# Kernel tuning notes

Hardware: AMD Instinct MI355X
Metric: run time of the kernel (lower is better)

Reference implementation:

```python
import jax, jax.numpy as jnp
import numpy as np

B, T, D = 2, 2048, 1024
H = 16
DH = D // H


def setup_inputs() -> dict:
    key = jax.random.key(0)
    ks = jax.random.split(key, 6)
    s = 1.0 / np.sqrt(D)
    return {
        "input_emb": jax.random.normal(ks[0], (B, T, D), dtype=jnp.float32),
        "W_key": jax.random.normal(ks[1], (D, D), dtype=jnp.float32) * s,
        "W_query": jax.random.normal(ks[2], (D, D), dtype=jnp.float32) * s,
        "W_value": jax.random.normal(ks[3], (D, D), dtype=jnp.float32) * s,
        "W_out": jax.random.normal(ks[4], (D, D), dtype=jnp.float32) * s,
        "b_out": jnp.zeros((D,), dtype=jnp.float32),
    }


def reference(input_emb, W_key, W_query, W_value, W_out, b_out):
    b, t, _ = input_emb.shape
    # projections (no bias on K/Q/V, matching bias_on=False)
    k = (input_emb @ W_key).reshape(b, t, H, DH).transpose(0, 2, 1, 3)    # [b,h,t,dh]
    q = (input_emb @ W_query).reshape(b, t, H, DH).transpose(0, 2, 1, 3)
    v = (input_emb @ W_value).reshape(b, t, H, DH).transpose(0, 2, 1, 3)
    # NOTE: source computes K @ Q^T (not Q @ K^T) — reproduce faithfully.
    scores = jnp.einsum("bhid,bhjd->bhij", k, q) / jnp.sqrt(jnp.float32(DH))
    mask = jnp.triu(jnp.ones((t, t), dtype=bool), k=1)                    # True where j > i
    scores = jnp.where(mask, -jnp.inf, scores)
    attn = jax.nn.softmax(scores, axis=-1)                                # softmax over j (query axis)
    ctx = jnp.einsum("bhij,bhjd->bhid", attn, v)                          # [b,h,t,dh]
    ctx = ctx.transpose(0, 2, 1, 3).reshape(b, t, H * DH)                 # [b,t,d]
    return ctx @ W_out + b_out
```

## Files before the change

kernel.cpp:

```cpp
#include <hip/hip_runtime.h>
#include <cstdint>
#include <cstddef>

#define T_SEQ 2048
#define DMODEL 1024
#define NHEAD 16
#define DHEAD 64
#define BATCH 2
#define MROWS (BATCH * T_SEQ)

typedef __attribute__((ext_vector_type(8))) short bf16x8;
typedef __attribute__((ext_vector_type(4))) float f32x4;
typedef unsigned int u32;

__device__ __forceinline__ unsigned short f2bf(float f) {
  u32 u = __float_as_uint(f);
  u32 r = (u + 0x7FFFu + ((u >> 16) & 1u)) >> 16;
  return (unsigned short)r;
}

__device__ __forceinline__ u32 cvtpk(float a, float b) {
  u32 r;
  asm("v_cvt_pk_bf16_f32 %0, %1, %2" : "=v"(r) : "v"(a), "v"(b));
  return r;
}

__device__ __forceinline__ void gl_lds16(const unsigned short* g, unsigned short* l) {
  __builtin_amdgcn_global_load_lds(
      (const __attribute__((address_space(1))) u32*)g,
      (__attribute__((address_space(3))) u32*)l, 16, 0, 0);
}

__global__ void k_prep(const float* __restrict__ X, unsigned short* __restrict__ Xb,
                       const float* __restrict__ W0, const float* __restrict__ W1,
                       const float* __restrict__ W2, const float* __restrict__ W3,
                       unsigned short* __restrict__ T0, unsigned short* __restrict__ T1,
                       unsigned short* __restrict__ T2, unsigned short* __restrict__ T3) {
  const int bid = blockIdx.x;
  if (bid < 4096) {
    int i = (bid * 256 + threadIdx.x) * 4;
    float4 v = *reinterpret_cast<const float4*>(X + i);
    ushort4 o;
    o.x = f2bf(v.x); o.y = f2bf(v.y); o.z = f2bf(v.z); o.w = f2bf(v.w);
    *reinterpret_cast<ushort4*>(Xb + i) = o;
    return;
  }
  const int b2 = bid - 4096;
  const int z = b2 >> 10;
  const int rem = b2 & 1023;
  const int cx = rem & 31, ry = rem >> 5;
  const float* W = (z == 0) ? W0 : (z == 1) ? W1 : (z == 2) ? W2 : W3;
  unsigned short* Wt = (z == 0) ? T0 : (z == 1) ? T1 : (z == 2) ? T2 : T3;
  __shared__ float tile[32][33];
  const int c0 = cx * 32, r0 = ry * 32;
  const int tx = threadIdx.x & 31, ty = threadIdx.x >> 5;
#pragma unroll
  for (int i = ty; i < 32; i += 8)
    tile[i][tx] = W[(size_t)(r0 + i) * DMODEL + c0 + tx];
  __syncthreads();
#pragma unroll
  for (int i = ty; i < 32; i += 8)
    Wt[(size_t)(c0 + i) * DMODEL + r0 + tx] = f2bf(tile[tx][i]);
}

__global__ __launch_bounds__(256, 2)
void k_gemm_qkv(const unsigned short* __restrict__ Xb,
                const unsigned short* __restrict__ Wkt,
                const unsigned short* __restrict__ Wqt,
                const unsigned short* __restrict__ Wvt,
                unsigned short* __restrict__ Qr,
                unsigned short* __restrict__ Kr,
                unsigned short* __restrict__ Vt)
{
  __shared__ __align__(16) unsigned short As[3][128 * 32];
  __shared__ __align__(16) unsigned short Bs[3][128 * 32];
  const int orig = blockIdx.x;
  const int t = (orig & 7) * 96 + (orig >> 3);
  const int z = t >> 8;
  const int remt = t & 255;
  const int by = remt >> 3, bx = remt & 7;
  const unsigned short* Bt = (z == 0) ? Wkt : (z == 1) ? Wqt : Wvt;

  const int tid = threadIdx.x;
  const int lane = tid & 63, w = tid >> 6;
  const int wr = w >> 1, wc = w & 1;
  const int l15 = lane & 15, l4 = lane >> 4;
  const int m0 = by * 128, n0 = bx * 128;

  const int srow = tid >> 2, scc = tid & 3;
  const unsigned short* Ab0 = Xb + (size_t)(m0 + srow) * DMODEL + scc * 8;
  const unsigned short* Bb0 = Bt + (size_t)(n0 + srow) * DMODEL + scc * 8;
  const unsigned short* Ab1 = Ab0 + (size_t)64 * DMODEL;
  const unsigned short* Bb1 = Bb0 + (size_t)64 * DMODEL;

#define GSTAGE(buf, koff)                                                 \
  {                                                                       \
    gl_lds16(Ab0 + (koff), As[buf] + tid * 8);                            \
    gl_lds16(Ab1 + (koff), As[buf] + 2048 + tid * 8);                     \
    gl_lds16(Bb0 + (koff), Bs[buf] + tid * 8);                            \
    gl_lds16(Bb1 + (koff), Bs[buf] + 2048 + tid * 8);                     \
  }

#define GCOMP(buf)                                                        \
  {                                                                       \
    bf16x8 af[4], bfr[4];                                                 \
    _Pragma("unroll")                                                     \
    for (int mi = 0; mi < 4; ++mi)                                        \
      af[mi] = *reinterpret_cast<const bf16x8*>(As[buf] + (wr * 64 + mi * 16 + l15) * 32 + l4 * 8); \
    _Pragma("unroll")                                                     \
    for (int ni = 0; ni < 4; ++ni)                                        \
      bfr[ni] = *reinterpret_cast<const bf16x8*>(Bs[buf] + (wc * 64 + ni * 16 + l15) * 32 + l4 * 8); \
    __builtin_amdgcn_s_setprio(1);                                        \
    _Pragma("unroll")                                                     \
    for (int mi = 0; mi < 4; ++mi)                                        \
      _Pragma("unroll")                                                   \
      for (int ni = 0; ni < 4; ++ni)                                      \
        acc[mi][ni] = __builtin_amdgcn_mfma_f32_16x16x32_bf16(af[mi], bfr[ni], acc[mi][ni], 0, 0, 0); \
    __builtin_amdgcn_s_setprio(0);                                        \
  }

#define SB __builtin_amdgcn_sched_barrier(0);
#define GW4 asm volatile("s_waitcnt vmcnt(4)" ::: "memory");
#define GW0 asm volatile("s_waitcnt vmcnt(0)" ::: "memory");

#define GSTEP(P, NB)                                                      \
  SB GW4 SB __builtin_amdgcn_s_barrier(); SB                              \
  if (ko < DMODEL) { GSTAGE(NB, ko) ko += 32; }                           \
  GCOMP(P)

  f32x4 acc[4][4] = {};

  GSTAGE(0, 0)
  GSTAGE(1, 32)
  int ko = 64;
  for (int j = 0; j < 10; ++j) {
    GSTEP(0, 2)
    GSTEP(1, 0)
    GSTEP(2, 1)
  }
  SB GW4 SB __builtin_amdgcn_s_barrier(); SB
  GCOMP(0)
  SB GW0 SB __builtin_amdgcn_s_barrier(); SB
  GCOMP(1)
#undef GSTEP
#undef GSTAGE
#undef GCOMP
#undef GW4
#undef GW0

  if (z < 2) {
    unsigned short* C = (z == 0) ? Qr : Kr;
#pragma unroll
    for (int mi = 0; mi < 4; ++mi)
#pragma unroll
      for (int ni = 0; ni < 4; ++ni) {
        const int col = n0 + wc * 64 + ni * 16 + l15;
        const int rowb = m0 + wr * 64 + mi * 16 + l4 * 4;
#pragma unroll
        for (int r = 0; r < 4; ++r)
          C[(size_t)(rowb + r) * DMODEL + col] = f2bf(acc[mi][ni][r]);
      }
  } else {
#pragma unroll
    for (int mi = 0; mi < 4; ++mi)
#pragma unroll
      for (int ni = 0; ni < 4; ++ni) {
        const int col = n0 + wc * 64 + ni * 16 + l15;
        const int h = col >> 6, dh = col & 63;
        const int rowb = m0 + wr * 64 + mi * 16 + l4 * 4;
        const int b = rowb >> 11, tt = rowb & (T_SEQ - 1);
        const int tl = tt & 63;
        const int tp = (tt & ~63) | (tl & 32) | ((tl & 12) << 1) | ((tl & 16) >> 2);
        unsigned short* p = Vt + ((size_t)(b * NHEAD + h) * DHEAD + dh) * T_SEQ + tp;
        ushort4 pkv;
        pkv.x = f2bf(acc[mi][ni][0]); pkv.y = f2bf(acc[mi][ni][1]);
        pkv.z = f2bf(acc[mi][ni][2]); pkv.w = f2bf(acc[mi][ni][3]);
        *reinterpret_cast<ushort4*>(p) = pkv;
      }
  }
}

__global__ __launch_bounds__(256, 2)
void k_attn(const unsigned short* __restrict__ Qr,
            const unsigned short* __restrict__ Kr,
            const unsigned short* __restrict__ Vp,
            unsigned short* __restrict__ ctx)
{
  __shared__ __align__(16) char lds[65536];
  const int tid = threadIdx.x;
  const int lane = tid & 63, w = tid >> 6;
  const int l15 = lane & 15, l4 = lane >> 4;

  const int x = blockIdx.x;
  const int xcd = x & 7, idx = x >> 3;
  const int bh = xcd + 8 * (idx & 3);
  const int cpair = idx >> 2;
  const int b = bh >> 4, h = bh & 15;

  const unsigned short* Qbase = Qr + (size_t)b * T_SEQ * DMODEL + h * DHEAD;
  const unsigned short* Kbase = Kr + (size_t)b * T_SEQ * DMODEL + h * DHEAD;
  const unsigned short* Vbase = Vp + (size_t)bh * DHEAD * T_SEQ;
  unsigned short* obase = ctx + (size_t)b * T_SEQ * DMODEL + h * DHEAD;

  const float SC = 0.18033688011112042f;
  const float M0 = 12.0f;
  const int srow = tid >> 3, scb = tid & 7;
  const int scolE = (scb ^ (srow & 7)) << 3;

  const int sw = (l15 & 7) << 4;
  const char* aK0 = lds + l15 * 128 + ((l4 * 16) ^ sw);
  const char* aK1 = lds + l15 * 128 + (((64 + l4 * 16)) ^ sw);

  const unsigned short* kp = Kbase + (size_t)srow * DMODEL + scolE;
  const unsigned short* vpb = Vbase + (size_t)srow * T_SEQ + scolE;

#define KRD(P, st, ni, v1) (*reinterpret_cast<const bf16x8*>(((v1) ? aK1 : aK0) + (P) * 16384 + (st) * 8192 + (ni) * 2048))
#define VRD(P, st, df, hk) (*reinterpret_cast<const bf16x8*>(((hk) ? aK1 : aK0) + 32768 + (P) * 16384 + (st) * 8192 + (df) * 2048))

#define STAGE(KD, VD, kg, vg)                                                     \
      {                                                                           \
        gl_lds16((kg), (KD) + tid * 8);                                           \
        gl_lds16((kg) + 32 * DMODEL, (KD) + 2048 + tid * 8);                      \
        gl_lds16((kg) + 64 * DMODEL, (KD) + 4096 + tid * 8);                      \
        gl_lds16((kg) + 96 * DMODEL, (KD) + 6144 + tid * 8);                      \
        gl_lds16((vg), (VD) + tid * 8);                                           \
        gl_lds16((vg) + 32 * T_SEQ, (VD) + 2048 + tid * 8);                       \
        gl_lds16((vg) + 64, (VD) + 4096 + tid * 8);                               \
        gl_lds16((vg) + 32 * T_SEQ + 64, (VD) + 6144 + tid * 8);                  \
      }

#define GROUP_BODY(g, P)                                                          \
    {                                                                             \
      const int kv0 = (g) * 128;                                                  \
      const bool diag = ((g) == NG - 1);                                          \
      __builtin_amdgcn_sched_barrier(0);                                          \
      asm volatile("s_waitcnt vmcnt(0)" ::: "memory");                            \
      __builtin_amdgcn_sched_barrier(0);                                          \
      __builtin_amdgcn_s_barrier();                                               \
      __builtin_amdgcn_sched_barrier(0);                                          \
      if ((g) + 1 < NG) {                                                         \
        unsigned short* Kn = (unsigned short*)(lds + ((P) ^ 1) * 16384);          \
        unsigned short* Vn = (unsigned short*)(lds + 32768 + ((P) ^ 1) * 16384);  \
        STAGE(Kn, Vn, kstage, vstage)                                             \
        kstage += 128 * DMODEL; vstage += 128;                                    \
      }                                                                           \
      __builtin_amdgcn_sched_barrier(0);                                          \
      const bool a1 = !diag || codd;                                              \
      const int nlim0 = (diag && !codd) ? (w + 1) : 4;                            \
      const int nlim1 = (diag && codd) ? (w + 1) : 4;                             \
      f32x4 S[2][4] = {};                                                         \
      __builtin_amdgcn_s_setprio(1);                                              \
      _Pragma("unroll")                                                           \
      for (int ni = 0; ni < 4; ++ni)                                              \
        if (ni < nlim0) {                                                         \
          S[0][ni] = __builtin_amdgcn_mfma_f32_16x16x32_bf16(KRD(P, 0, ni, 0), qf[0], S[0][ni], 0, 0, 0); \
          S[0][ni] = __builtin_amdgcn_mfma_f32_16x16x32_bf16(KRD(P, 0, ni, 1), qf[1], S[0][ni], 0, 0, 0); \
        }                                                                         \
      if (a1) {                                                                   \
        _Pragma("unroll")                                                         \
        for (int ni = 0; ni < 4; ++ni)                                            \
          if (ni < nlim1) {                                                       \
            S[1][ni] = __builtin_amdgcn_mfma_f32_16x16x32_bf16(KRD(P, 1, ni, 0), qf[0], S[1][ni], 0, 0, 0); \
            S[1][ni] = __builtin_amdgcn_mfma_f32_16x16x32_bf16(KRD(P, 1, ni, 1), qf[1], S[1][ni], 0, 0, 0); \
          }                                                                       \
      }                                                                           \
      __builtin_amdgcn_s_setprio(0);                                              \
      if (diag) {                                                                 \
        if (!codd) {                                                              \
          _Pragma("unroll")                                                       \
          for (int ni = 0; ni < 4; ++ni)                                          \
            if (ni < nlim0) {                                                     \
              _Pragma("unroll")                                                   \
              for (int r = 0; r < 4; ++r)                                         \
                if (kv0 + ni * 16 + l4 * 4 + r > qrow) S[0][ni][r] = -INFINITY;   \
            }                                                                     \
        } else {                                                                  \
          _Pragma("unroll")                                                       \
          for (int ni = 0; ni < 4; ++ni)                                          \
            if (ni < nlim1) {                                                     \
              _Pragma("unroll")                                                   \
              for (int r = 0; r < 4; ++r)                                         \
                if (kv0 + 64 + ni * 16 + l4 * 4 + r > qrow) S[1][ni][r] = -INFINITY; \
            }                                                                     \
        }                                                                         \
      }                                                                           \
      union __align__(16) PW { u32 u[2][2][4]; bf16x8 v[2][2]; } pw = {};         \
      _Pragma("unroll")                                                           \
      for (int ni = 0; ni < 4; ++ni)                                              \
        if (ni < nlim0) {                                                         \
          const float p0 = __builtin_amdgcn_exp2f(__builtin_fmaf(S[0][ni][0], SC, -M0)); \
          const float p1 = __builtin_amdgcn_exp2f(__builtin_fmaf(S[0][ni][1], SC, -M0)); \
          const float p2 = __builtin_amdgcn_exp2f(__builtin_fmaf(S[0][ni][2], SC, -M0)); \
          const float p3 = __builtin_amdgcn_exp2f(__builtin_fmaf(S[0][ni][3], SC, -M0)); \
          lP += (p0 + p1) + (p2 + p3);                                            \
          pw.u[0][ni >> 1][(ni & 1) * 2]     = cvtpk(p0, p1);                     \
          pw.u[0][ni >> 1][(ni & 1) * 2 + 1] = cvtpk(p2, p3);                     \
        }                                                                         \
      if (a1) {                                                                   \
        _Pragma("unroll")                                                         \
        for (int ni = 0; ni < 4; ++ni)                                            \
          if (ni < nlim1) {                                                       \
            const float p0 = __builtin_amdgcn_exp2f(__builtin_fmaf(S[1][ni][0], SC, -M0)); \
            const float p1 = __builtin_amdgcn_exp2f(__builtin_fmaf(S[1][ni][1], SC, -M0)); \
            const float p2 = __builtin_amdgcn_exp2f(__builtin_fmaf(S[1][ni][2], SC, -M0)); \
            const float p3 = __builtin_amdgcn_exp2f(__builtin_fmaf(S[1][ni][3], SC, -M0)); \
            lP += (p0 + p1) + (p2 + p3);                                          \
            pw.u[1][ni >> 1][(ni & 1) * 2]     = cvtpk(p0, p1);                   \
            pw.u[1][ni >> 1][(ni & 1) * 2 + 1] = cvtpk(p2, p3);                   \
          }                                                                       \
      }                                                                           \
      __builtin_amdgcn_s_setprio(1);                                              \
      {                                                                           \
        const int hkl0 = (diag && !codd) ? ((nlim0 + 1) >> 1) : 2;                \
        _Pragma("unroll")                                                         \
        for (int hk = 0; hk < 2; ++hk)                                            \
          if (hk < hkl0) {                                                        \
            _Pragma("unroll")                                                     \
            for (int df = 0; df < 4; ++df)                                        \
              O[df] = __builtin_amdgcn_mfma_f32_16x16x32_bf16(VRD(P, 0, df, hk), pw.v[0][hk], O[df], 0, 0, 0); \
          }                                                                       \
      }                                                                           \
      if (a1) {                                                                   \
        const int hkl1 = (diag && codd) ? ((nlim1 + 1) >> 1) : 2;                 \
        _Pragma("unroll")                                                         \
        for (int hk = 0; hk < 2; ++hk)                                            \
          if (hk < hkl1) {                                                        \
            _Pragma("unroll")                                                     \
            for (int df = 0; df < 4; ++df)                                        \
              O[df] = __builtin_amdgcn_mfma_f32_16x16x32_bf16(VRD(P, 1, df, hk), pw.v[1][hk], O[df], 0, 0, 0); \
          }                                                                       \
      }                                                                           \
      __builtin_amdgcn_s_setprio(0);                                              \
      __builtin_amdgcn_sched_barrier(0);                                          \
    }

  for (int half = 0; half < 2; ++half) {
    const int c = half ? (31 - cpair) : cpair;
    const bool codd = (c & 1) != 0;
    const int q0w = c * 64 + w * 16;
    const int NG = (c + 2) >> 1;
    const int qrow = q0w + l15;

    bf16x8 qf[2];
#pragma unroll
    for (int ks = 0; ks < 2; ++ks)
      qf[ks] = *reinterpret_cast<const bf16x8*>(
          Qbase + (size_t)(q0w + l15) * DMODEL + ks * 32 + l4 * 8);

    __builtin_amdgcn_sched_barrier(0);
    __builtin_amdgcn_s_barrier();
    __builtin_amdgcn_sched_barrier(0);
    {
      unsigned short* Ks = (unsigned short*)(lds);
      unsigned short* Vs = (unsigned short*)(lds + 32768);
      STAGE(Ks, Vs, kp, vpb)
    }
    const unsigned short* kstage = kp + 128 * DMODEL;
    const unsigned short* vstage = vpb + 128;

    f32x4 O[4] = {};
    float lP = 0.f;

    for (int g2 = 0; g2 < NG; g2 += 2) {
      GROUP_BODY(g2, 0)
      if (g2 + 1 < NG) GROUP_BODY(g2 + 1, 1)
    }

    float lS = lP;
    lS += __shfl_xor(lS, 16);
    lS += __shfl_xor(lS, 32);
    const float rinv = 1.0f / lS;
#pragma unroll
    for (int df = 0; df < 4; ++df) {
      ushort4 o;
      o.x = f2bf(O[df][0] * rinv);
      o.y = f2bf(O[df][1] * rinv);
      o.z = f2bf(O[df][2] * rinv);
      o.w = f2bf(O[df][3] * rinv);
      *reinterpret_cast<ushort4*>(obase + (size_t)qrow * DMODEL + df * 16 + l4 * 4) = o;
    }
  }
#undef GROUP_BODY
#undef STAGE
#undef KRD
#undef VRD
}

__global__ __launch_bounds__(256, 2)
void k_gemm_out(const unsigned short* __restrict__ Ab,
                const unsigned short* __restrict__ Bt,
                const float* __restrict__ bias,
                float* __restrict__ C)
{
  __shared__ __align__(16) unsigned short As[3][128 * 32];
  __shared__ __align__(16) unsigned short Bs[3][128 * 32];
  const int orig = blockIdx.x;
  const int t = (orig & 7) * 32 + (orig >> 3);
  const int by = t >> 3, bx = t & 7;

  const int tid = threadIdx.x;
  const int lane = tid & 63, w = tid >> 6;
  const int wr = w >> 1, wc = w & 1;
  const int l15 = lane & 15, l4 = lane >> 4;
  const int m0 = by * 128, n0 = bx * 128;

  const int srow = tid >> 2, scc = tid & 3;
  const unsigned short* Ab0 = Ab + (size_t)(m0 + srow) * DMODEL + scc * 8;
  const unsigned short* Bb0 = Bt + (size_t)(n0 + srow) * DMODEL + scc * 8;
  const unsigned short* Ab1 = Ab0 + (size_t)64 * DMODEL;
  const unsigned short* Bb1 = Bb0 + (size_t)64 * DMODEL;

#define GSTAGE(buf, koff)                                                 \
  {                                                                       \
    gl_lds16(Ab0 + (koff), As[buf] + tid * 8);                            \
    gl_lds16(Ab1 + (koff), As[buf] + 2048 + tid * 8);                     \
    gl_lds16(Bb0 + (koff), Bs[buf] + tid * 8);                            \
    gl_lds16(Bb1 + (koff), Bs[buf] + 2048 + tid * 8);                     \
  }

#define GCOMP(buf)                                                        \
  {                                                                       \
    bf16x8 af[4], bfr[4];                                                 \
    _Pragma("unroll")                                                     \
    for (int mi = 0; mi < 4; ++mi)                                        \
      af[mi] = *reinterpret_cast<const bf16x8*>(As[buf] + (wr * 64 + mi * 16 + l15) * 32 + l4 * 8); \
    _Pragma("unroll")                                                     \
    for (int ni = 0; ni < 4; ++ni)                                        \
      bfr[ni] = *reinterpret_cast<const bf16x8*>(Bs[buf] + (wc * 64 + ni * 16 + l15) * 32 + l4 * 8); \
    __builtin_amdgcn_s_setprio(1);                                        \
    _Pragma("unroll")                                                     \
    for (int mi = 0; mi < 4; ++mi)                                        \
      _Pragma("unroll")                                                   \
      for (int ni = 0; ni < 4; ++ni)                                      \
        acc[mi][ni] = __builtin_amdgcn_mfma_f32_16x16x32_bf16(af[mi], bfr[ni], acc[mi][ni], 0, 0, 0); \
    __builtin_amdgcn_s_setprio(0);                                        \
  }

#define GW4 asm volatile("s_waitcnt vmcnt(4)" ::: "memory");
#define GW0 asm volatile("s_waitcnt vmcnt(0)" ::: "memory");

#define GSTEP(P, NB)                                                      \
  SB GW4 SB __builtin_amdgcn_s_barrier(); SB                              \
  if (ko < DMODEL) { GSTAGE(NB, ko) ko += 32; }                           \
  GCOMP(P)

  f32x4 acc[4][4] = {};

  GSTAGE(0, 0)
  GSTAGE(1, 32)
  int ko = 64;
  for (int j = 0; j < 10; ++j) {
    GSTEP(0, 2)
    GSTEP(1, 0)
    GSTEP(2, 1)
  }
  SB GW4 SB __builtin_amdgcn_s_barrier(); SB
  GCOMP(0)
  SB GW0 SB __builtin_amdgcn_s_barrier(); SB
  GCOMP(1)
#undef GSTEP
#undef GSTAGE
#undef GCOMP
#undef GW4
#undef GW0
#undef SB

#pragma unroll
  for (int mi = 0; mi < 4; ++mi)
#pragma unroll
    for (int ni = 0; ni < 4; ++ni) {
      const int col = n0 + wc * 64 + ni * 16 + l15;
      const float bv = bias[col];
      const int rowb = m0 + wr * 64 + mi * 16 + l4 * 4;
#pragma unroll
      for (int r = 0; r < 4; ++r)
        C[(size_t)(rowb + r) * DMODEL + col] = acc[mi][ni][r] + bv;
    }
}

extern "C" void kernel_launch(void* const* d_in, const int* in_sizes, int n_in,
                              void* d_out, int out_size, void* d_ws, size_t ws_size,
                              hipStream_t stream) {
  const float* X  = (const float*)d_in[0];
  const float* Wk = (const float*)d_in[1];
  const float* Wq = (const float*)d_in[2];
  const float* Wv = (const float*)d_in[3];
  const float* Wo = (const float*)d_in[4];
  const float* bo = (const float*)d_in[5];
  float* out = (float*)d_out;

  char* ws = (char*)d_ws;
  const size_t MB = 1024 * 1024;
  unsigned short* Xb  = (unsigned short*)(ws + 0 * MB);
  unsigned short* Wkt = (unsigned short*)(ws + 8 * MB);
  unsigned short* Wqt = (unsigned short*)(ws + 10 * MB);
  unsigned short* Wvt = (unsigned short*)(ws + 12 * MB);
  unsigned short* Wot = (unsigned short*)(ws + 14 * MB);
  unsigned short* Qr  = (unsigned short*)(ws + 16 * MB);
  unsigned short* Kr  = (unsigned short*)(ws + 24 * MB);
  unsigned short* Vt  = (unsigned short*)(ws + 32 * MB);
  unsigned short* Ctx = (unsigned short*)(ws + 40 * MB);

  k_prep<<<8192, 256, 0, stream>>>(X, Xb, Wk, Wq, Wv, Wo, Wkt, Wqt, Wvt, Wot);
  k_gemm_qkv<<<768, 256, 0, stream>>>(Xb, Wkt, Wqt, Wvt, Qr, Kr, Vt);
  k_attn<<<dim3(512), 256, 0, stream>>>(Qr, Kr, Vt, Ctx);
  k_gemm_out<<<256, 256, 0, stream>>>(Ctx, Wot, bo, out);
}
```

Before: 102.7 us.

## Widen attention query tile to 128 rows per block with two row-groups per wave

After: 109.3 us. +6.4%, slower.

```diff
diff --git a/kernel.cpp b/kernel.cpp
--- a/kernel.cpp
+++ b/kernel.cpp
@@ -12,6 +12,8 @@
 typedef __attribute__((ext_vector_type(8))) short bf16x8;
 typedef __attribute__((ext_vector_type(4))) float f32x4;
 typedef unsigned int u32;
+
+#define SB __builtin_amdgcn_sched_barrier(0);
 
 __device__ __forceinline__ unsigned short f2bf(float f) {
   u32 u = __float_as_uint(f);
@@ -119,7 +121,6 @@
     __builtin_amdgcn_s_setprio(0);                                        \
   }
 
-#define SB __builtin_amdgcn_sched_barrier(0);
 #define GW4 asm volatile("s_waitcnt vmcnt(4)" ::: "memory");
 #define GW0 asm volatile("s_waitcnt vmcnt(0)" ::: "memory");
 
@@ -192,9 +193,11 @@
   const int l15 = lane & 15, l4 = lane >> 4;
 
   const int x = blockIdx.x;
-  const int xcd = x & 7, idx = x >> 3;
+  const int ph = x >> 8, j = x & 255;
+  const int xcd = j & 7, idx = j >> 3;
   const int bh = xcd + 8 * (idx & 3);
-  const int cpair = idx >> 2;
+  const int c0 = idx >> 2;
+  const int c = ph ? (15 - c0) : c0;
   const int b = bh >> 4, h = bh & 15;
 
   const unsigned short* Qbase = Qr + (size_t)b * T_SEQ * DMODEL + h * DHEAD;
@@ -214,6 +217,14 @@
   const unsigned short* kp = Kbase + (size_t)srow * DMODEL + scolE;
   const unsigned short* vpb = Vbase + (size_t)srow * T_SEQ + scolE;
 
+  const int q0w = c * 128 + w * 32;
+  const int NG = c + 1;
+  const int qrow0 = q0w + l15;
+  const int qrow1 = q0w + 16 + l15;
+
+  union __align__(16) PW { u32 u[2][4]; bf16x8 v[2]; };
+
+#define MFMA(a, bq, cc) __builtin_amdgcn_mfma_f32_16x16x32_bf16((a), (bq), (cc), 0, 0, 0)
 #define KRD(P, st, ni, v1) (*reinterpret_cast<const bf16x8*>(((v1) ? aK1 : aK0) + (P) * 16384 + (st) * 8192 + (ni) * 2048))
 #define VRD(P, st, df, hk) (*reinterpret_cast<const bf16x8*>(((hk) ? aK1 : aK0) + 32768 + (P) * 16384 + (st) * 8192 + (df) * 2048))
 
@@ -233,157 +244,202 @@
     {                                                                             \
       const int kv0 = (g) * 128;                                                  \
       const bool diag = ((g) == NG - 1);                                          \
-      __builtin_amdgcn_sched_barrier(0);                                          \
-      asm volatile("s_waitcnt vmcnt(0)" ::: "memory");                            \
-      __builtin_amdgcn_sched_barrier(0);                                          \
-      __builtin_amdgcn_s_barrier();                                               \
-      __builtin_amdgcn_sched_barrier(0);                                          \
+      SB asm volatile("s_waitcnt vmcnt(0)" ::: "memory"); SB                      \
+      __builtin_amdgcn_s_barrier(); SB                                            \
       if ((g) + 1 < NG) {                                                         \
         unsigned short* Kn = (unsigned short*)(lds + ((P) ^ 1) * 16384);          \
         unsigned short* Vn = (unsigned short*)(lds + 32768 + ((P) ^ 1) * 16384);  \
         STAGE(Kn, Vn, kstage, vstage)                                             \
         kstage += 128 * DMODEL; vstage += 128;                                    \
       }                                                                           \
-      __builtin_amdgcn_sched_barrier(0);                                          \
-      const bool a1 = !diag || codd;                                              \
-      const int nlim0 = (diag && !codd) ? (w + 1) : 4;                            \
-      const int nlim1 = (diag && codd) ? (w + 1) : 4;                             \
-      f32x4 S[2][4] = {};                                                         \
+      SB                                                                          \
+      int nl00 = 4, nl01 = 4, nl10 = 4, nl11 = 4;                                 \
+      if (diag) {                                                                 \
+        nl00 = 2 * w + 1; if (nl00 > 4) nl00 = 4;                                 \
+        nl01 = 2 * w + 2; if (nl01 > 4) nl01 = 4;                                 \
+        nl10 = ((32 * w - 49) >> 4) + 1; if (nl10 < 0) nl10 = 0;                  \
+        nl11 = ((32 * w - 33) >> 4) + 1; if (nl11 < 0) nl11 = 0;                  \
+      }                                                                           \
+      const bool a1 = !diag || (w >= 2);                                          \
+      f32x4 S[2][2][4] = {};                                                      \
       __builtin_amdgcn_s_setprio(1);                                              \
       _Pragma("unroll")                                                           \
       for (int ni = 0; ni < 4; ++ni)                                              \
-        if (ni < nlim0) {                                                         \
-          S[0][ni] = __builtin_amdgcn_mfma_f32_16x16x32_bf16(KRD(P, 0, ni, 0), qf[0], S[0][ni], 0, 0, 0); \
-          S[0][ni] = __builtin_amdgcn_mfma_f32_16x16x32_bf16(KRD(P, 0, ni, 1), qf[1], S[0][ni], 0, 0, 0); \
+        if (ni < nl01) {                                                          \
+          const bf16x8 ka = KRD(P, 0, ni, 0);                                     \
+          const bf16x8 kb = KRD(P, 0, ni, 1);                                     \
+          if (ni < nl00) {                                                        \
+            S[0][0][ni] = MFMA(ka, qf[0][0], S[0][0][ni]);                        \
+            S[0][0][ni] = MFMA(kb, qf[0][1], S[0][0][ni]);                        \
+          }                                                                       \
+          S[0][1][ni] = MFMA(ka, qf[1][0], S[0][1][ni]);                          \
+          S[0][1][ni] = MFMA(kb, qf[1][1], S[0][1][ni]);                          \
         }                                                                         \
       if (a1) {                                                                   \
         _Pragma("unroll")                                                         \
         for (int ni = 0; ni < 4; ++ni)                                            \
-          if (ni < nlim1) {                                                       \
-            S[1][ni] = __builtin_amdgcn_mfma_f32_16x16x32_bf16(KRD(P, 1, ni, 0), qf[0], S[1][ni], 0, 0, 0); \
-            S[1][ni] = __builtin_amdgcn_mfma_f32_16x16x32_bf16(KRD(P, 1, ni, 1), qf[1], S[1][ni], 0, 0, 0); \
+          if (ni < nl11) {                                                        \
+            const bf16x8 ka = KRD(P, 1, ni, 0);                                   \
+            const bf16x8 kb = KRD(P, 1, ni, 1);                                   \
+            if (ni < nl10) {                                                      \
+              S[1][0][ni] = MFMA(ka, qf[0][0], S[1][0][ni]);                      \
+              S[1][0][ni] = MFMA(kb, qf[0][1], S[1][0][ni]);                      \
+            }                                                                     \
+            S[1][1][ni] = MFMA(ka, qf[1][0], S[1][1][ni]);                        \
+            S[1][1][ni] = MFMA(kb, qf[1][1], S[1][1][ni]);                        \
           }                                                                       \
       }                                                                           \
       __builtin_amdgcn_s_setprio(0);                                              \
       if (diag) {                                                                 \
-        if (!codd) {                                                              \
-          _Pragma("unroll")                                                       \
-          for (int ni = 0; ni < 4; ++ni)                                          \
-            if (ni < nlim0) {                                                     \
-              _Pragma("unroll")                                                   \
-              for (int r = 0; r < 4; ++r)                                         \
-                if (kv0 + ni * 16 + l4 * 4 + r > qrow) S[0][ni][r] = -INFINITY;   \
-            }                                                                     \
-        } else {                                                                  \
-          _Pragma("unroll")                                                       \
-          for (int ni = 0; ni < 4; ++ni)                                          \
-            if (ni < nlim1) {                                                     \
-              _Pragma("unroll")                                                   \
-              for (int r = 0; r < 4; ++r)                                         \
-                if (kv0 + 64 + ni * 16 + l4 * 4 + r > qrow) S[1][ni][r] = -INFINITY; \
-            }                                                                     \
+        _Pragma("unroll")                                                         \
+        for (int ni = 0; ni < 4; ++ni) {                                          \
+          if (ni < nl00) {                                                        \
+            _Pragma("unroll")                                                     \
+            for (int r = 0; r < 4; ++r)                                           \
+              if (kv0 + ni * 16 + l4 * 4 + r > qrow0) S[0][0][ni][r] = -INFINITY; \
+          }                                                                       \
+          if (ni < nl01) {                                                        \
+            _Pragma("unroll")                                                     \
+            for (int r = 0; r < 4; ++r)                                           \
+              if (kv0 + ni * 16 + l4 * 4 + r > qrow1) S[0][1][ni][r] = -INFINITY; \
+          }                                                                       \
+          if (ni < nl10) {                                                        \
+            _Pragma("unroll")                                                     \
+            for (int r = 0; r < 4; ++r)                                           \
+              if (kv0 + 64 + ni * 16 + l4 * 4 + r > qrow0) S[1][0][ni][r] = -INFINITY; \
+          }                                                                       \
+          if (ni < nl11) {                                                        \
+            _Pragma("unroll")                                                     \
+            for (int r = 0; r < 4; ++r)                                           \
+              if (kv0 + 64 + ni * 16 + l4 * 4 + r > qrow1) S[1][1][ni][r] = -INFINITY; \
+          }                                                                       \
         }                                                                         \
       }                                                                           \
-      union __align__(16) PW { u32 u[2][2][4]; bf16x8 v[2][2]; } pw = {};         \
+      PW pw00 = {}, pw01 = {}, pw10 = {}, pw11 = {};                              \
       _Pragma("unroll")                                                           \
-      for (int ni = 0; ni < 4; ++ni)                                              \
-        if (ni < nlim0) {                                                         \
-          const float p0 = __builtin_amdgcn_exp2f(__builtin_fmaf(S[0][ni][0], SC, -M0)); \
-          const float p1 = __builtin_amdgcn_exp2f(__builtin_fmaf(S[0][ni][1], SC, -M0)); \
-          const float p2 = __builtin_amdgcn_exp2f(__builtin_fmaf(S[0][ni][2], SC, -M0)); \
-          const float p3 = __builtin_amdgcn_exp2f(__builtin_fmaf(S[0][ni][3], SC, -M0)); \
-          lP += (p0 + p1) + (p2 + p3);                                            \
-          pw.u[0][ni >> 1][(ni & 1) * 2]     = cvtpk(p0, p1);                     \
-          pw.u[0][ni >> 1][(ni & 1) * 2 + 1] = cvtpk(p2, p3);                     \
+      for (int ni = 0; ni < 4; ++ni) {                                            \
+        if (ni < nl00) {                                                          \
+          const float p0 = __builtin_amdgcn_exp2f(__builtin_fmaf(S[0][0][ni][0], SC, -M0)); \
+          const float p1 = __builtin_amdgcn_exp2f(__builtin_fmaf(S[0][0][ni][1], SC, -M0)); \
+          const float p2 = __builtin_amdgcn_exp2f(__builtin_fmaf(S[0][0][ni][2], SC, -M0)); \
+          const float p3 = __builtin_amdgcn_exp2f(__builtin_fmaf(S[0][0][ni][3], SC, -M0)); \
+          lP0 += (p0 + p1) + (p2 + p3);                                           \
+          pw00.u[ni >> 1][(ni & 1) * 2]     = cvtpk(p0, p1);                      \
+          pw00.u[ni >> 1][(ni & 1) * 2 + 1] = cvtpk(p2, p3);                      \
         }                                                                         \
+        if (ni < nl01) {                                                          \
+          const float p0 = __builtin_amdgcn_exp2f(__builtin_fmaf(S[0][1][ni][0], SC, -M0)); \
+          const float p1 = __builtin_amdgcn_exp2f(__builtin_fmaf(S[0][1][ni][1], SC, -M0)); \
+          const float p2 = __builtin_amdgcn_exp2f(__builtin_fmaf(S[0][1][ni][2], SC, -M0)); \
+          const float p3 = __builtin_amdgcn_exp2f(__builtin_fmaf(S[0][1][ni][3], SC, -M0)); \
+          lP1 += (p0 + p1) + (p2 + p3);                                           \
+          pw01.u[ni >> 1][(ni & 1) * 2]     = cvtpk(p0, p1);                      \
+          pw01.u[ni >> 1][(ni & 1) * 2 + 1] = cvtpk(p2, p3);                      \
+        }                                                                         \
+      }                                                                           \
       if (a1) {                                                                   \
         _Pragma("unroll")                                                         \
-        for (int ni = 0; ni < 4; ++ni)                                            \
-          if (ni < nlim1) {                                                       \
-            const float p0 = __builtin_amdgcn_exp2f(__builtin_fmaf(S[1][ni][0], SC, -M0)); \
-            const float p1 = __builtin_amdgcn_exp2f(__builtin_fmaf(S[1][ni][1], SC, -M0)); \
-            const float p2 = __builtin_amdgcn_exp2f(__builtin_fmaf(S[1][ni][2], SC, -M0)); \
-            const float p3 = __builtin_amdgcn_exp2f(__builtin_fmaf(S[1][ni][3], SC, -M0)); \
-            lP += (p0 + p1) + (p2 + p3);                                          \
-            pw.u[1][ni >> 1][(ni & 1) * 2]     = cvtpk(p0, p1);                   \
-            pw.u[1][ni >> 1][(ni & 1) * 2 + 1] = cvtpk(p2, p3);                   \
-          }                                                                       \
+        for (int ni = 0; ni < 4; ++ni) {                                          \
+          if (ni < nl10) {                                                        \
+            const float p0 = __builtin_amdgcn_exp2f(__builtin_fmaf(S[1][0][ni][0], SC, -M0)); \
+            const float p1 = __builtin_amdgcn_exp2f(__builtin_fmaf(S[1][0][ni][1], SC, -M0)); \
+            const float p2 = __builtin_amdgcn_exp2f(__builtin_fmaf(S[1][0][ni][2], SC, -M0)); \
+            const float p3 = __builtin_amdgcn_exp2f(__builtin_fmaf(S[1][0][ni][3], SC, -M0)); \
+            lP0 += (p0 + p1) + (p2 + p3);                                         \
+            pw10.u[ni >> 1][(ni & 1) * 2]     = cvtpk(p0, p1);                    \
+            pw10.u[ni >> 1][(ni & 1) * 2 + 1] = cvtpk(p2, p3);                    \
+          }                                                                       \
+          if (ni < nl11) {                                                        \
+            const float p0 = __builtin_amdgcn_exp2f(__builtin_fmaf(S[1][1][ni][0], SC, -M0)); \
+            const float p1 = __builtin_amdgcn_exp2f(__builtin_fmaf(S[1][1][ni][1], SC, -M0)); \
+            const float p2 = __builtin_amdgcn_exp2f(__builtin_fmaf(S[1][1][ni][2], SC, -M0)); \
+            const float p3 = __builtin_amdgcn_exp2f(__builtin_fmaf(S[1][1][ni][3], SC, -M0)); \
+            lP1 += (p0 + p1) + (p2 + p3);                                         \
+            pw11.u[ni >> 1][(ni & 1) * 2]     = cvtpk(p0, p1);                    \
+            pw11.u[ni >> 1][(ni & 1) * 2 + 1] = cvtpk(p2, p3);                    \
+          }                                                                       \
+        }                                                                         \
       }                                                                           \
       __builtin_amdgcn_s_setprio(1);                                              \
       {                                                                           \
-        const int hkl0 = (diag && !codd) ? ((nlim0 + 1) >> 1) : 2;                \
+        const int hkl0 = diag ? ((nl01 + 1) >> 1) : 2;                            \
         _Pragma("unroll")                                                         \
         for (int hk = 0; hk < 2; ++hk)                                            \
           if (hk < hkl0) {                                                        \
             _Pragma("unroll")                                                     \
-            for (int df = 0; df < 4; ++df)                                        \
-              O[df] = __builtin_amdgcn_mfma_f32_16x16x32_bf16(VRD(P, 0, df, hk), pw.v[0][hk], O[df], 0, 0, 0); \
+            for (int df = 0; df < 4; ++df) {                                      \
+              const bf16x8 vv = VRD(P, 0, df, hk);                                \
+              O0[df] = MFMA(vv, pw00.v[hk], O0[df]);                              \
+              O1[df] = MFMA(vv, pw01.v[hk], O1[df]);                              \
+            }                                                                     \
           }                                                                       \
       }                                                                           \
       if (a1) {                                                                   \
-        const int hkl1 = (diag && codd) ? ((nlim1 + 1) >> 1) : 2;                 \
+        const int hkl1 = diag ? ((nl11 + 1) >> 1) : 2;                            \
         _Pragma("unroll")                                                         \
         for (int hk = 0; hk < 2; ++hk)                                            \
           if (hk < hkl1) {                                                        \
             _Pragma("unroll")                                                     \
-            for (int df = 0; df < 4; ++df)                                        \
-              O[df] = __builtin_amdgcn_mfma_f32_16x16x32_bf16(VRD(P, 1, df, hk), pw.v[1][hk], O[df], 0, 0, 0); \
+            for (int df = 0; df < 4; ++df) {                                      \
+              const bf16x8 vv = VRD(P, 1, df, hk);                                \
+              O0[df] = MFMA(vv, pw10.v[hk], O0[df]);                              \
+              O1[df] = MFMA(vv, pw11.v[hk], O1[df]);                              \
+            }                                                                     \
           }                                                                       \
       }                                                                           \
       __builtin_amdgcn_s_setprio(0);                                              \
-      __builtin_amdgcn_sched_barrier(0);                                          \
+      SB                                                                          \
     }
 
-  for (int half = 0; half < 2; ++half) {
-    const int c = half ? (31 - cpair) : cpair;
-    const bool codd = (c & 1) != 0;
-    const int q0w = c * 64 + w * 16;
-    const int NG = (c + 2) >> 1;
-    const int qrow = q0w + l15;
-
-    bf16x8 qf[2];
+  bf16x8 qf[2][2];
+#pragma unroll
+  for (int qm = 0; qm < 2; ++qm)
 #pragma unroll
     for (int ks = 0; ks < 2; ++ks)
-      qf[ks] = *reinterpret_cast<const bf16x8*>(
-          Qbase + (size_t)(q0w + l15) * DMODEL + ks * 32 + l4 * 8);
-
-    __builtin_amdgcn_sched_barrier(0);
-    __builtin_amdgcn_s_barrier();
-    __builtin_amdgcn_sched_barrier(0);
-    {
-      unsigned short* Ks = (unsigned short*)(lds);
-      unsigned short* Vs = (unsigned short*)(lds + 32768);
-      STAGE(Ks, Vs, kp, vpb)
-    }
-    const unsigned short* kstage = kp + 128 * DMODEL;
-    const unsigned short* vstage = vpb + 128;
-
-    f32x4 O[4] = {};
-    float lP = 0.f;
-
-    for (int g2 = 0; g2 < NG; g2 += 2) {
-      GROUP_BODY(g2, 0)
-      if (g2 + 1 < NG) GROUP_BODY(g2 + 1, 1)
-    }
-
-    float lS = lP;
-    lS += __shfl_xor(lS, 16);
-    lS += __shfl_xor(lS, 32);
-    const float rinv = 1.0f / lS;
+      qf[qm][ks] = *reinterpret_cast<const bf16x8*>(
+          Qbase + (size_t)(q0w + qm * 16 + l15) * DMODEL + ks * 32 + l4 * 8);
+
+  {
+    unsigned short* Ks = (unsigned short*)(lds);
+    unsigned short* Vs = (unsigned short*)(lds + 32768);
+    STAGE(Ks, Vs, kp, vpb)
+  }
+  const unsigned short* kstage = kp + 128 * DMODEL;
+  const unsigned short* vstage = vpb + 128;
+
+  f32x4 O0[4] = {}, O1[4] = {};
+  float lP0 = 0.f, lP1 = 0.f;
+
+  for (int g2 = 0; g2 < NG; g2 += 2) {
+    GROUP_BODY(g2, 0)
+    if (g2 + 1 < NG) GROUP_BODY(g2 + 1, 1)
+  }
+
+  {
+    float lS0 = lP0;
+    lS0 += __shfl_xor(lS0, 16);
+    lS0 += __shfl_xor(lS0, 32);
+    float lS1 = lP1;
+    lS1 += __shfl_xor(lS1, 16);
+    lS1 += __shfl_xor(lS1, 32);
+    const float rinv0 = 1.0f / lS0;
+    const float rinv1 = 1.0f / lS1;
 #pragma unroll
     for (int df = 0; df < 4; ++df) {
-      ushort4 o;
-      o.x = f2bf(O[df][0] * rinv);
-      o.y = f2bf(O[df][1] * rinv);
-      o.z = f2bf(O[df][2] * rinv);
-      o.w = f2bf(O[df][3] * rinv);
-      *reinterpret_cast<ushort4*>(obase + (size_t)qrow * DMODEL + df * 16 + l4 * 4) = o;
+      ushort4 o0, o1;
+      o0.x = f2bf(O0[df][0] * rinv0); o0.y = f2bf(O0[df][1] * rinv0);
+      o0.z = f2bf(O0[df][2] * rinv0); o0.w = f2bf(O0[df][3] * rinv0);
+      o1.x = f2bf(O1[df][0] * rinv1); o1.y = f2bf(O1[df][1] * rinv1);
+      o1.z = f2bf(O1[df][2] * rinv1); o1.w = f2bf(O1[df][3] * rinv1);
+      *reinterpret_cast<ushort4*>(obase + (size_t)qrow0 * DMODEL + df * 16 + l4 * 4) = o0;
+      *reinterpret_cast<ushort4*>(obase + (size_t)qrow1 * DMODEL + df * 16 + l4 * 4) = o1;
     }
   }
 #undef GROUP_BODY
 #undef STAGE
 #undef KRD
 #undef VRD
+#undef MFMA
 }
 
 __global__ __launch_bounds__(256, 2)
@@ -463,7 +519,6 @@
 #undef GCOMP
 #undef GW4
 #undef GW0
-#undef SB
 
 #pragma unroll
   for (int mi = 0; mi < 4; ++mi)
```
